# Kernel tuning notes

Hardware: AMD Instinct MI355X
Metric: run time of the kernel (lower is better)

Reference implementation:

```python
import jax, jax.numpy as jnp
import numpy as np

LOG2 = 0.6931471805599453
GAMMA = 10.0
NUM_KERNELS = 301
N_LAYERS = 3


def ssp(v):
    # ShiftedSoftplus: softplus(x) - log(2)
    return jax.nn.softplus(v) - jnp.asarray(LOG2, v.dtype)


def setup_inputs() -> dict:
    key = jax.random.key(0)
    ks = jax.random.split(key, 20)
    N, F, K, L, V = 512, 128, NUM_KERNELS, N_LAYERS, 100
    s = 0.05
    return {
        "x": jax.random.randint(ks[0], (N,), 0, V),
        "r": jax.random.uniform(ks[1], (N, 3), dtype=jnp.float32) * 10.0,
        "emb": jax.random.normal(ks[2], (V, F), dtype=jnp.float32),
        "aw_W": jax.random.normal(ks[3], (L, F, F), dtype=jnp.float32) * s,
        "aw_b": jax.random.normal(ks[4], (L, F), dtype=jnp.float32) * s,
        "cf_W1": jax.random.normal(ks[5], (L, K, F), dtype=jnp.float32) * s,
        "cf_b1": jax.random.normal(ks[6], (L, F), dtype=jnp.float32) * s,
        "cf_W2": jax.random.normal(ks[7], (L, F, F), dtype=jnp.float32) * s,
        "cf_b2": jax.random.normal(ks[8], (L, F), dtype=jnp.float32) * s,
        "n_W1": jax.random.normal(ks[9], (L, F, F), dtype=jnp.float32) * s,
        "n_b1": jax.random.normal(ks[10], (L, F), dtype=jnp.float32) * s,
        "n_W2": jax.random.normal(ks[11], (L, F, F), dtype=jnp.float32) * s,
        "n_b2": jax.random.normal(ks[12], (L, F), dtype=jnp.float32) * s,
        "out_W1": jax.random.normal(ks[13], (F, 32), dtype=jnp.float32) * s,
        "out_b1": jax.random.normal(ks[14], (32,), dtype=jnp.float32) * s,
        "out_W2": jax.random.normal(ks[15], (32, 1), dtype=jnp.float32) * s,
        "out_b2": jax.random.normal(ks[16], (1,), dtype=jnp.float32) * s,
    }


def reference(x, r, emb, aw_W, aw_b, cf_W1, cf_b1, cf_W2, cf_b2,
              n_W1, n_b1, n_W2, n_b2, out_W1, out_b1, out_W2, out_b2):
    centers = jnp.linspace(0.0, 30.0, NUM_KERNELS, dtype=r.dtype)  # [K]
    # pairwise distances (torch.cdist, p=2) with safe sqrt at the diagonal
    diff = r[:, None, :] - r[None, :, :]                 # [N,N,3]
    d2 = jnp.sum(diff * diff, axis=-1)                   # [N,N]
    mask = d2 > 0
    d = jnp.where(mask, jnp.sqrt(jnp.where(mask, d2, 1.0)), 0.0)

    h = emb[x]                                           # [N,F]
    for l in range(N_LAYERS):
        o = h @ aw_W[l] + aw_b[l]                        # atom-wise linear
        # Gaussian RBF expansion: [N,N,K]
        e = jnp.exp(-GAMMA * jnp.square(d[..., None] - centers))
        # filter-generating MLP: [N,N,F]
        w = ssp(e @ cf_W1[l] + cf_b1[l])
        w = ssp(w @ cf_W2[l] + cf_b2[l])
        # continuous-filter conv: o[i,k] = sum_j x[j,k] * w[i,j,k]
        c = jnp.einsum('jk,ijk->ik', o, w)
        c = ssp(c @ n_W1[l] + n_b1[l]) @ n_W2[l] + n_b2[l]
        h = h + c
    out = ssp(h @ out_W1 + out_b1) @ out_W2 + out_b2     # [N,1]
    # AdaptiveAvgPool1d(1) on a 2D [N,1] tensor is identity over L=1
    return out.reshape(-1)
```

## Files before the change

kernel.cpp:

```cpp
#include <hip/hip_runtime.h>
#include <hip/hip_fp16.h>
#include <math.h>

#define N_ATOMS 512
#define F_DIM   128
#define K_RBF   301
#define NLAYER  3
#define GAMMA_C 10.0f
#define LOG2_C  0.6931471805599453f

#define TAB_H    0.01f
#define TAB_INVH 100.0f
#define TAB_ROWS 1768
#define RPB      8

__device__ __forceinline__ float ssp(float x) {
    float ax = fabsf(x);
    return fmaxf(x, 0.0f) + log1pf(expf(-ax)) - LOG2_C;
}

__global__ void prep_kernel(const int* __restrict__ x, const float* __restrict__ r,
                            const float* __restrict__ emb,
                            const float* __restrict__ aw_W, const float* __restrict__ aw_b,
                            float* __restrict__ dmat, float* __restrict__ h,
                            float* __restrict__ o) {
    int i = blockIdx.x;
    int t = threadIdx.x;
    __shared__ float hs[F_DIM];
    float rx = r[i * 3 + 0], ry = r[i * 3 + 1], rz = r[i * 3 + 2];
    if (t < F_DIM) {
        float hv = emb[x[i] * F_DIM + t];
        h[i * F_DIM + t] = hv;
        hs[t] = hv;
    }
    for (int j = t; j < N_ATOMS; j += 256) {
        float dx = rx - r[j * 3 + 0];
        float dy = ry - r[j * 3 + 1];
        float dz = rz - r[j * 3 + 2];
        dmat[i * N_ATOMS + j] = sqrtf(dx * dx + dy * dy + dz * dz);
    }
    __syncthreads();
    if (t < F_DIM) {
        float acc = aw_b[t];
        for (int g = 0; g < F_DIM; ++g) acc = fmaf(hs[g], aw_W[g * F_DIM + t], acc);
        o[i * F_DIM + t] = acc;
    }
}

__global__ void build_tables(const float* __restrict__ cf_W1, const float* __restrict__ cf_b1,
                             const float* __restrict__ cf_W2, const float* __restrict__ cf_b2,
                             float* __restrict__ tab) {
    int row0 = blockIdx.x * RPB;
    int l    = blockIdx.y;
    int f    = threadIdx.x;

    float dlo = row0 * TAB_H;
    float dhi = (row0 + RPB - 1) * TAB_H;
    int k0 = ::max(0, (int)ceilf((dlo - 1.45f) * 10.0f));
    int k1 = ::min(K_RBF - 1, (int)floorf((dhi + 1.45f) * 10.0f));
    int kw = k1 - k0 + 1;

    __shared__ float e_s[RPB][40];
    __shared__ float w1_s[F_DIM][RPB];

    for (int idx = f; idx < RPB * kw; idx += F_DIM) {
        int rr = idx / kw, kk = idx % kw;
        float dv = (row0 + rr) * TAB_H;
        float tt = dv - 0.1f * (float)(k0 + kk);
        e_s[rr][kk] = expf(-GAMMA_C * tt * tt);
    }
    __syncthreads();

    const float* W1 = cf_W1 + l * K_RBF * F_DIM;
    float b1v = cf_b1[l * F_DIM + f];
    float acc[RPB];
#pragma unroll
    for (int rr = 0; rr < RPB; ++rr) acc[rr] = b1v;
    for (int kk = 0; kk < kw; ++kk) {
        float w1v = W1[(k0 + kk) * F_DIM + f];
#pragma unroll
        for (int rr = 0; rr < RPB; ++rr) acc[rr] = fmaf(e_s[rr][kk], w1v, acc[rr]);
    }
    {
        float4 s0, s1;
        s0.x = ssp(acc[0]); s0.y = ssp(acc[1]); s0.z = ssp(acc[2]); s0.w = ssp(acc[3]);
        s1.x = ssp(acc[4]); s1.y = ssp(acc[5]); s1.z = ssp(acc[6]); s1.w = ssp(acc[7]);
        *(float4*)&w1_s[f][0] = s0;
        *(float4*)&w1_s[f][4] = s1;
    }
    __syncthreads();

    const float* W2 = cf_W2 + l * F_DIM * F_DIM;
    float b2v = cf_b2[l * F_DIM + f];
    float acc2[RPB];
#pragma unroll
    for (int rr = 0; rr < RPB; ++rr) acc2[rr] = b2v;
    for (int g = 0; g < F_DIM; ++g) {
        float w2v = W2[g * F_DIM + f];
        float4 wa = *(const float4*)&w1_s[g][0];
        float4 wb = *(const float4*)&w1_s[g][4];
        acc2[0] = fmaf(wa.x, w2v, acc2[0]);
        acc2[1] = fmaf(wa.y, w2v, acc2[1]);
        acc2[2] = fmaf(wa.z, w2v, acc2[2]);
        acc2[3] = fmaf(wa.w, w2v, acc2[3]);
        acc2[4] = fmaf(wb.x, w2v, acc2[4]);
        acc2[5] = fmaf(wb.y, w2v, acc2[5]);
        acc2[6] = fmaf(wb.z, w2v, acc2[6]);
        acc2[7] = fmaf(wb.w, w2v, acc2[7]);
    }
#pragma unroll
    for (int rr = 0; rr < RPB; ++rr)
        tab[(l * TAB_ROWS + row0 + rr) * F_DIM + f] = ssp(acc2[rr]);
}

__global__ void pack_tables(const float* __restrict__ tab, __half2* __restrict__ ptab) {
    int idx = blockIdx.x * 256 + threadIdx.x;
    int total = NLAYER * TAB_ROWS * F_DIM;
    if (idx >= total) return;
    int row = (idx / F_DIM) % TAB_ROWS;
    float t0 = tab[idx];
    float t1 = (row < TAB_ROWS - 1) ? tab[idx + F_DIM] : t0;
    ptab[idx] = __halves2half2(__float2half(t0), __float2half(t1 - t0));
}

__global__ void __launch_bounds__(512)
conv_kernel(const float* __restrict__ dmat, const float* __restrict__ o,
            const __half2* __restrict__ ptab, float* __restrict__ c, int l) {
    int i  = blockIdx.x;
    int t  = threadIdx.x;
    int f  = t & (F_DIM - 1);
    int jc = t >> 7;

    __shared__ float ds[N_ATOMS];
    __shared__ float red[4][F_DIM];

    for (int j = t; j < N_ATOMS; j += 512) ds[j] = dmat[i * N_ATOMS + j];
    __syncthreads();

    const __half2* T = ptab + l * TAB_ROWS * F_DIM;
    float acc = 0.0f;
#pragma unroll 4
    for (int jj = 0; jj < N_ATOMS / 4; ++jj) {
        int j = jc * (N_ATOMS / 4) + jj;
        float dv = ds[j];
        float xb = dv * TAB_INVH;
        int   b  = ::min((int)xb, TAB_ROWS - 2);
        float fr = xb - (float)b;
        __half2 tv = T[b * F_DIM + f];
        float t0 = __half2float(__low2half(tv));
        float dt = __half2float(__high2half(tv));
        float w  = fmaf(fr, dt, t0);
        acc = fmaf(w, o[j * F_DIM + f], acc);
    }
    red[jc][f] = acc;
    __syncthreads();
    if (jc == 0) {
        c[i * F_DIM + f] = red[0][f] + red[1][f] + red[2][f] + red[3][f];
    }
}

__global__ void node_fused(const float* __restrict__ c, const float* __restrict__ n_W1,
                           const float* __restrict__ n_b1, const float* __restrict__ n_W2,
                           const float* __restrict__ n_b2, float* __restrict__ h,
                           const float* __restrict__ aw_W, const float* __restrict__ aw_b,
                           float* __restrict__ o,
                           const float* __restrict__ oW1, const float* __restrict__ ob1,
                           const float* __restrict__ oW2, const float* __restrict__ ob2,
                           float* __restrict__ out, int l) {
    int i = blockIdx.x, f = threadIdx.x;
    __shared__ float cs[F_DIM];
    __shared__ float t1s[F_DIM];
    __shared__ float hs[F_DIM];
    cs[f] = c[i * F_DIM + f];
    __syncthreads();
    const float* W1 = n_W1 + l * F_DIM * F_DIM;
    float a = n_b1[l * F_DIM + f];
    for (int g = 0; g < F_DIM; ++g) a = fmaf(cs[g], W1[g * F_DIM + f], a);
    t1s[f] = ssp(a);
    __syncthreads();
    const float* W2 = n_W2 + l * F_DIM * F_DIM;
    float a2 = n_b2[l * F_DIM + f];
    for (int g = 0; g < F_DIM; ++g) a2 = fmaf(t1s[g], W2[g * F_DIM + f], a2);
    float hv = h[i * F_DIM + f] + a2;
    h[i * F_DIM + f] = hv;
    hs[f] = hv;
    __syncthreads();

    if (l < NLAYER - 1) {
        const float* W = aw_W + (l + 1) * F_DIM * F_DIM;
        float acc = aw_b[(l + 1) * F_DIM + f];
        for (int g = 0; g < F_DIM; ++g) acc = fmaf(hs[g], W[g * F_DIM + f], acc);
        o[i * F_DIM + f] = acc;
    } else {
        float val = 0.0f;
        if (f < 32) {
            float ah = ob1[f];
            for (int g = 0; g < F_DIM; ++g) ah = fmaf(hs[g], oW1[g * 32 + f], ah);
            val = ssp(ah) * oW2[f];
        }
#pragma unroll
        for (int off = 16; off > 0; off >>= 1) val += __shfl_xor(val, off, 64);
        if (f == 0) out[i] = val + ob2[0];
    }
}

extern "C" void kernel_launch(void* const* d_in, const int* in_sizes, int n_in,
                              void* d_out, int out_size, void* d_ws, size_t ws_size,
                              hipStream_t stream) {
    const int*   x     = (const int*)  d_in[0];
    const float* r     = (const float*)d_in[1];
    const float* emb   = (const float*)d_in[2];
    const float* aw_W  = (const float*)d_in[3];
    const float* aw_b  = (const float*)d_in[4];
    const float* cf_W1 = (const float*)d_in[5];
    const float* cf_b1 = (const float*)d_in[6];
    const float* cf_W2 = (const float*)d_in[7];
    const float* cf_b2 = (const float*)d_in[8];
    const float* n_W1  = (const float*)d_in[9];
    const float* n_b1  = (const float*)d_in[10];
    const float* n_W2  = (const float*)d_in[11];
    const float* n_b2  = (const float*)d_in[12];
    const float* oW1   = (const float*)d_in[13];
    const float* ob1   = (const float*)d_in[14];
    const float* oW2   = (const float*)d_in[15];
    const float* ob2   = (const float*)d_in[16];
    float* out = (float*)d_out;

    char* ws = (char*)d_ws;
    float*   dmat = (float*)ws;   ws += (size_t)N_ATOMS * N_ATOMS * 4;
    float*   h    = (float*)ws;   ws += (size_t)N_ATOMS * F_DIM * 4;
    float*   o    = (float*)ws;   ws += (size_t)N_ATOMS * F_DIM * 4;
    float*   c    = (float*)ws;   ws += (size_t)N_ATOMS * F_DIM * 4;
    float*   tab  = (float*)ws;   ws += (size_t)NLAYER * TAB_ROWS * F_DIM * 4;
    __half2* ptab = (__half2*)ws;

    prep_kernel<<<N_ATOMS, 256, 0, stream>>>(x, r, emb, aw_W, aw_b, dmat, h, o);
    build_tables<<<dim3(TAB_ROWS / RPB, NLAYER), 128, 0, stream>>>(cf_W1, cf_b1, cf_W2, cf_b2, tab);
    {
        int total = NLAYER * TAB_ROWS * F_DIM;
        pack_tables<<<(total + 255) / 256, 256, 0, stream>>>(tab, ptab);
    }
    for (int l = 0; l < NLAYER; ++l) {
        conv_kernel<<<N_ATOMS, 512, 0, stream>>>(dmat, o, ptab, c, l);
        node_fused<<<N_ATOMS, 128, 0, stream>>>(c, n_W1, n_b1, n_W2, n_b2, h,
                                                aw_W, aw_b, o, oW1, ob1, oW2, ob2, out, l);
    }
}
```

Baseline: 191.4 us.

## Pack table, distances and o in half precision, fuse table packing into build

Distances are precomputed as a table byte offset plus a half-precision fraction. The o activations are stored as packed half2. The interpolation table is built directly in packed form, with value and delta for two features per entry, so the separate pack kernel is gone. The conv kernel now has each thread handle two features, uses half2 FMA for interpolation and loads fewer bytes per j. This trades precision (o and the fraction are now fp16) for less memory traffic and fewer index computations in the hot loop, and it drops one launch.

After: 175.2 us. 1.09x faster.

```diff
diff --git a/kernel.cpp b/kernel.cpp
--- a/kernel.cpp
+++ b/kernel.cpp
@@ -9,24 +9,32 @@
 #define GAMMA_C 10.0f
 #define LOG2_C  0.6931471805599453f
 
-#define TAB_H    0.01f
-#define TAB_INVH 100.0f
-#define TAB_ROWS 1768
-#define RPB      8
+#define TAB_H     0.01f
+#define TAB_INVH  100.0f
+#define TAB_ROWS  1768
+#define RPB       8
+#define ROW_BYTES 512
 
 __device__ __forceinline__ float ssp(float x) {
     float ax = fabsf(x);
     return fmaxf(x, 0.0f) + log1pf(expf(-ax)) - LOG2_C;
 }
+__device__ __forceinline__ __half2 u2h2(unsigned u) {
+    union { unsigned u; __half2 h; } c; c.u = u; return c.h;
+}
+__device__ __forceinline__ unsigned h22u(__half2 h) {
+    union { unsigned u; __half2 h; } c; c.h = h; return c.u;
+}
 
 __global__ void prep_kernel(const int* __restrict__ x, const float* __restrict__ r,
                             const float* __restrict__ emb,
                             const float* __restrict__ aw_W, const float* __restrict__ aw_b,
-                            float* __restrict__ dmat, float* __restrict__ h,
-                            float* __restrict__ o) {
+                            uint2* __restrict__ dpk, float* __restrict__ h,
+                            unsigned* __restrict__ opk) {
     int i = blockIdx.x;
     int t = threadIdx.x;
     __shared__ float hs[F_DIM];
+    __shared__ float os[F_DIM];
     float rx = r[i * 3 + 0], ry = r[i * 3 + 1], rz = r[i * 3 + 2];
     if (t < F_DIM) {
         float hv = emb[x[i] * F_DIM + t];
@@ -37,33 +45,44 @@
         float dx = rx - r[j * 3 + 0];
         float dy = ry - r[j * 3 + 1];
         float dz = rz - r[j * 3 + 2];
-        dmat[i * N_ATOMS + j] = sqrtf(dx * dx + dy * dy + dz * dz);
+        float d  = sqrtf(dx * dx + dy * dy + dz * dz);
+        float xb = d * TAB_INVH;
+        int   b  = ::min((int)xb, TAB_ROWS - 2);
+        float fr = xb - (float)b;
+        __half fh = __float2half(fr);
+        dpk[i * N_ATOMS + j] = make_uint2((unsigned)b * ROW_BYTES,
+                                          h22u(__halves2half2(fh, fh)));
     }
     __syncthreads();
     if (t < F_DIM) {
         float acc = aw_b[t];
         for (int g = 0; g < F_DIM; ++g) acc = fmaf(hs[g], aw_W[g * F_DIM + t], acc);
-        o[i * F_DIM + t] = acc;
-    }
+        os[t] = acc;
+    }
+    __syncthreads();
+    if (t < F_DIM / 2)
+        opk[i * 64 + t] = h22u(__halves2half2(__float2half(os[2 * t]),
+                                              __float2half(os[2 * t + 1])));
 }
 
 __global__ void build_tables(const float* __restrict__ cf_W1, const float* __restrict__ cf_b1,
                              const float* __restrict__ cf_W2, const float* __restrict__ cf_b2,
-                             float* __restrict__ tab) {
+                             uint2* __restrict__ ptab) {
     int row0 = blockIdx.x * RPB;
     int l    = blockIdx.y;
     int f    = threadIdx.x;
 
     float dlo = row0 * TAB_H;
-    float dhi = (row0 + RPB - 1) * TAB_H;
+    float dhi = (row0 + RPB) * TAB_H;
     int k0 = ::max(0, (int)ceilf((dlo - 1.45f) * 10.0f));
     int k1 = ::min(K_RBF - 1, (int)floorf((dhi + 1.45f) * 10.0f));
     int kw = k1 - k0 + 1;
 
-    __shared__ float e_s[RPB][40];
-    __shared__ float w1_s[F_DIM][RPB];
-
-    for (int idx = f; idx < RPB * kw; idx += F_DIM) {
+    __shared__ float e_s[RPB + 1][34];
+    __shared__ float w1_s[F_DIM][12];
+    __shared__ float outs[RPB + 1][F_DIM];
+
+    for (int idx = f; idx < (RPB + 1) * kw; idx += F_DIM) {
         int rr = idx / kw, kk = idx % kw;
         float dv = (row0 + rr) * TAB_H;
         float tt = dv - 0.1f * (float)(k0 + kk);
@@ -73,32 +92,28 @@
 
     const float* W1 = cf_W1 + l * K_RBF * F_DIM;
     float b1v = cf_b1[l * F_DIM + f];
-    float acc[RPB];
-#pragma unroll
-    for (int rr = 0; rr < RPB; ++rr) acc[rr] = b1v;
+    float acc[RPB + 1];
+#pragma unroll
+    for (int rr = 0; rr <= RPB; ++rr) acc[rr] = b1v;
     for (int kk = 0; kk < kw; ++kk) {
         float w1v = W1[(k0 + kk) * F_DIM + f];
 #pragma unroll
-        for (int rr = 0; rr < RPB; ++rr) acc[rr] = fmaf(e_s[rr][kk], w1v, acc[rr]);
-    }
-    {
-        float4 s0, s1;
-        s0.x = ssp(acc[0]); s0.y = ssp(acc[1]); s0.z = ssp(acc[2]); s0.w = ssp(acc[3]);
-        s1.x = ssp(acc[4]); s1.y = ssp(acc[5]); s1.z = ssp(acc[6]); s1.w = ssp(acc[7]);
-        *(float4*)&w1_s[f][0] = s0;
-        *(float4*)&w1_s[f][4] = s1;
-    }
+        for (int rr = 0; rr <= RPB; ++rr) acc[rr] = fmaf(e_s[rr][kk], w1v, acc[rr]);
+    }
+#pragma unroll
+    for (int rr = 0; rr <= RPB; ++rr) w1_s[f][rr] = ssp(acc[rr]);
     __syncthreads();
 
     const float* W2 = cf_W2 + l * F_DIM * F_DIM;
     float b2v = cf_b2[l * F_DIM + f];
-    float acc2[RPB];
-#pragma unroll
-    for (int rr = 0; rr < RPB; ++rr) acc2[rr] = b2v;
+    float acc2[RPB + 1];
+#pragma unroll
+    for (int rr = 0; rr <= RPB; ++rr) acc2[rr] = b2v;
     for (int g = 0; g < F_DIM; ++g) {
         float w2v = W2[g * F_DIM + f];
         float4 wa = *(const float4*)&w1_s[g][0];
         float4 wb = *(const float4*)&w1_s[g][4];
+        float  wc = w1_s[g][8];
         acc2[0] = fmaf(wa.x, w2v, acc2[0]);
         acc2[1] = fmaf(wa.y, w2v, acc2[1]);
         acc2[2] = fmaf(wa.z, w2v, acc2[2]);
@@ -107,55 +122,60 @@
         acc2[5] = fmaf(wb.y, w2v, acc2[5]);
         acc2[6] = fmaf(wb.z, w2v, acc2[6]);
         acc2[7] = fmaf(wb.w, w2v, acc2[7]);
-    }
-#pragma unroll
-    for (int rr = 0; rr < RPB; ++rr)
-        tab[(l * TAB_ROWS + row0 + rr) * F_DIM + f] = ssp(acc2[rr]);
-}
-
-__global__ void pack_tables(const float* __restrict__ tab, __half2* __restrict__ ptab) {
-    int idx = blockIdx.x * 256 + threadIdx.x;
-    int total = NLAYER * TAB_ROWS * F_DIM;
-    if (idx >= total) return;
-    int row = (idx / F_DIM) % TAB_ROWS;
-    float t0 = tab[idx];
-    float t1 = (row < TAB_ROWS - 1) ? tab[idx + F_DIM] : t0;
-    ptab[idx] = __halves2half2(__float2half(t0), __float2half(t1 - t0));
+        acc2[8] = fmaf(wc,   w2v, acc2[8]);
+    }
+#pragma unroll
+    for (int rr = 0; rr <= RPB; ++rr) outs[rr][f] = ssp(acc2[rr]);
+    __syncthreads();
+
+    int p = f & 63;
+    int rbase = (f >> 6) * (RPB / 2);
+#pragma unroll
+    for (int q = 0; q < RPB / 2; ++q) {
+        int rr = rbase + q;
+        float t00 = outs[rr][2 * p],     t01 = outs[rr][2 * p + 1];
+        float n00 = outs[rr + 1][2 * p], n01 = outs[rr + 1][2 * p + 1];
+        uint2 v = make_uint2(
+            h22u(__halves2half2(__float2half(t00), __float2half(t01))),
+            h22u(__halves2half2(__float2half(n00 - t00), __float2half(n01 - t01))));
+        ptab[((size_t)l * TAB_ROWS + row0 + rr) * 64 + p] = v;
+    }
 }
 
 __global__ void __launch_bounds__(512)
-conv_kernel(const float* __restrict__ dmat, const float* __restrict__ o,
-            const __half2* __restrict__ ptab, float* __restrict__ c, int l) {
+conv_kernel(const uint2* __restrict__ dpk, const unsigned* __restrict__ opk,
+            const uint2* __restrict__ ptab, float* __restrict__ c, int l) {
     int i  = blockIdx.x;
     int t  = threadIdx.x;
-    int f  = t & (F_DIM - 1);
-    int jc = t >> 7;
-
-    __shared__ float ds[N_ATOMS];
-    __shared__ float red[4][F_DIM];
-
-    for (int j = t; j < N_ATOMS; j += 512) ds[j] = dmat[i * N_ATOMS + j];
-    __syncthreads();
-
-    const __half2* T = ptab + l * TAB_ROWS * F_DIM;
-    float acc = 0.0f;
+    int p  = t & 63;
+    int jc = t >> 6;
+
+    __shared__ uint2  ds[N_ATOMS];
+    __shared__ float2 red[8][64];
+
+    ds[t] = dpk[i * N_ATOMS + t];
+    __syncthreads();
+
+    const char* T = (const char*)(ptab + (size_t)l * TAB_ROWS * 64) + p * 8;
+    float2 acc = make_float2(0.0f, 0.0f);
+    int j = jc * 64;
 #pragma unroll 4
-    for (int jj = 0; jj < N_ATOMS / 4; ++jj) {
-        int j = jc * (N_ATOMS / 4) + jj;
-        float dv = ds[j];
-        float xb = dv * TAB_INVH;
-        int   b  = ::min((int)xb, TAB_ROWS - 2);
-        float fr = xb - (float)b;
-        __half2 tv = T[b * F_DIM + f];
-        float t0 = __half2float(__low2half(tv));
-        float dt = __half2float(__high2half(tv));
-        float w  = fmaf(fr, dt, t0);
-        acc = fmaf(w, o[j * F_DIM + f], acc);
-    }
-    red[jc][f] = acc;
+    for (int jj = 0; jj < 64; ++jj, ++j) {
+        uint2 e = ds[j];
+        __half2 fr2 = u2h2(e.y);
+        uint2 tv = *(const uint2*)(T + e.x);
+        __half2 w2 = __hfma2(fr2, u2h2(tv.y), u2h2(tv.x));
+        __half2 oh = u2h2(opk[j * 64 + p]);
+        acc.x = fmaf(__half2float(__low2half(w2)),  __half2float(__low2half(oh)),  acc.x);
+        acc.y = fmaf(__half2float(__high2half(w2)), __half2float(__high2half(oh)), acc.y);
+    }
+    red[jc][p] = acc;
     __syncthreads();
     if (jc == 0) {
-        c[i * F_DIM + f] = red[0][f] + red[1][f] + red[2][f] + red[3][f];
+        float2 s = red[0][p];
+#pragma unroll
+        for (int q = 1; q < 8; ++q) { s.x += red[q][p].x; s.y += red[q][p].y; }
+        *(float2*)&c[i * F_DIM + 2 * p] = s;
     }
 }
 
@@ -163,7 +183,7 @@
                            const float* __restrict__ n_b1, const float* __restrict__ n_W2,
                            const float* __restrict__ n_b2, float* __restrict__ h,
                            const float* __restrict__ aw_W, const float* __restrict__ aw_b,
-                           float* __restrict__ o,
+                           unsigned* __restrict__ opk,
                            const float* __restrict__ oW1, const float* __restrict__ ob1,
                            const float* __restrict__ oW2, const float* __restrict__ ob2,
                            float* __restrict__ out, int l) {
@@ -190,7 +210,11 @@
         const float* W = aw_W + (l + 1) * F_DIM * F_DIM;
         float acc = aw_b[(l + 1) * F_DIM + f];
         for (int g = 0; g < F_DIM; ++g) acc = fmaf(hs[g], W[g * F_DIM + f], acc);
-        o[i * F_DIM + f] = acc;
+        t1s[f] = acc;
+        __syncthreads();
+        if (f < F_DIM / 2)
+            opk[i * 64 + f] = h22u(__halves2half2(__float2half(t1s[2 * f]),
+                                                  __float2half(t1s[2 * f + 1])));
     } else {
         float val = 0.0f;
         if (f < 32) {
@@ -227,22 +251,17 @@
     float* out = (float*)d_out;
 
     char* ws = (char*)d_ws;
-    float*   dmat = (float*)ws;   ws += (size_t)N_ATOMS * N_ATOMS * 4;
-    float*   h    = (float*)ws;   ws += (size_t)N_ATOMS * F_DIM * 4;
-    float*   o    = (float*)ws;   ws += (size_t)N_ATOMS * F_DIM * 4;
-    float*   c    = (float*)ws;   ws += (size_t)N_ATOMS * F_DIM * 4;
-    float*   tab  = (float*)ws;   ws += (size_t)NLAYER * TAB_ROWS * F_DIM * 4;
-    __half2* ptab = (__half2*)ws;
-
-    prep_kernel<<<N_ATOMS, 256, 0, stream>>>(x, r, emb, aw_W, aw_b, dmat, h, o);
-    build_tables<<<dim3(TAB_ROWS / RPB, NLAYER), 128, 0, stream>>>(cf_W1, cf_b1, cf_W2, cf_b2, tab);
-    {
-        int total = NLAYER * TAB_ROWS * F_DIM;
-        pack_tables<<<(total + 255) / 256, 256, 0, stream>>>(tab, ptab);
-    }
+    uint2*    dpk  = (uint2*)ws;    ws += (size_t)N_ATOMS * N_ATOMS * 8;
+    float*    h    = (float*)ws;    ws += (size_t)N_ATOMS * F_DIM * 4;
+    unsigned* opk  = (unsigned*)ws; ws += (size_t)N_ATOMS * (F_DIM / 2) * 4;
+    float*    c    = (float*)ws;    ws += (size_t)N_ATOMS * F_DIM * 4;
+    uint2*    ptab = (uint2*)ws;
+
+    prep_kernel<<<N_ATOMS, 256, 0, stream>>>(x, r, emb, aw_W, aw_b, dpk, h, opk);
+    build_tables<<<dim3(TAB_ROWS / RPB, NLAYER), 128, 0, stream>>>(cf_W1, cf_b1, cf_W2, cf_b2, ptab);
     for (int l = 0; l < NLAYER; ++l) {
-        conv_kernel<<<N_ATOMS, 512, 0, stream>>>(dmat, o, ptab, c, l);
+        conv_kernel<<<N_ATOMS, 512, 0, stream>>>(dpk, opk, ptab, c, l);
         node_fused<<<N_ATOMS, 128, 0, stream>>>(c, n_W1, n_b1, n_W2, n_b2, h,
-                                                aw_W, aw_b, o, oW1, ob1, oW2, ob2, out, l);
-    }
-}
+                                                aw_W, aw_b, opk, oW1, ob1, oW2, ob2, out, l);
+    }
+}
```
